# Kernel optimization log

Hardware: AMD Instinct MI355X
Metric: run time of the kernel (lower is better)

Reference implementation:

```python
import jax, jax.numpy as jnp
import numpy as np

GRID = 64
BIG = 1.0e6  # threshold pushing masked-out pixels to huge distance


def _grid_dist(grid_h, grid_w):
    # pairwise euclidean distance between all grid points, (H, W, H, W)
    xs, ys = jnp.meshgrid(jnp.arange(grid_h), jnp.arange(grid_w), indexing='ij')
    coords = jnp.stack([xs.ravel(), ys.ravel()], axis=-1).astype(jnp.float32)  # (H*W, 2)
    d = jnp.sqrt(jnp.sum((coords[:, None, :] - coords[None, :, :]) ** 2, axis=-1))
    return d.reshape(grid_h, grid_w, grid_h, grid_w)


def setup_inputs() -> dict:
    key = jax.random.key(0)
    k1, k2 = jax.random.split(key)
    gt = jax.random.uniform(k1, (8, 64, 64), dtype=jnp.float32)
    pred = jax.random.uniform(k2, (8, 64, 64), dtype=jnp.float32)
    return {"gt": gt, "pred": pred}


def reference(gt, pred):
    # mode='l2_sq': sum over last axis (W for a (B,H,W) mask), then mean
    loss = jnp.mean(jnp.sum((gt - pred) ** 2, axis=-1))

    # affinity loss (dist_mat += 1.0 as in the original)
    dist = _grid_dist(GRID, GRID) + 1.0  # (64,64,64,64)

    gt_th = gt + (1.0 - gt) * BIG      # (B,H,W)
    pred_th = pred + (1.0 - pred) * BIG

    # dist_masked[b,h,w,i,j] = gt_th[b,h,w] * dist[h,w,i,j] * pred[b,i,j]
    dist_masked = gt_th[:, :, :, None, None] * dist[None] * pred[:, None, None, :, :]
    min_dist = jnp.mean(jnp.min(dist_masked, axis=(3, 4)))

    dist_masked_inv = pred_th[:, :, :, None, None] * dist[None] * gt[:, None, None, :, :]
    min_dist_inv = jnp.mean(jnp.min(dist_masked_inv, axis=(3, 4)))

    return (loss, min_dist, min_dist_inv)
```

## Files before the change

### kernel.cpp

```cpp
#include <hip/hip_runtime.h>

#define BIGV 1.0e6f

__global__ __launch_bounds__(64) void imageloss_bnb(
    const float* __restrict__ gt, const float* __restrict__ pred,
    float* __restrict__ ws, float* __restrict__ out)
{
    __shared__ float img[4096];
    __shared__ float tmin[64];
    __shared__ int   order[64];
    __shared__ int   cnt9[16];

    const int blk   = blockIdx.x;
    const int patch = blk & 63;
    const int dir   = (blk >> 6) & 1;
    const int b     = blk >> 7;
    const int lane  = threadIdx.x;

    const float* __restrict__ src = (dir ? gt : pred) + b * 4096;

    #pragma unroll
    for (int k = 0; k < 16; ++k)
        ((float4*)img)[k * 64 + lane] = ((const float4*)src)[k * 64 + lane];
    if (lane < 16) cnt9[lane] = 0;
    __syncthreads();

    const int ti = lane >> 3, tj = lane & 7;
    {
        const float* tp = img + ti * 512 + tj * 8;
        float tv = 1e30f;
        #pragma unroll
        for (int r = 0; r < 8; ++r) {
            float4 a = *(const float4*)(tp + r * 64);
            float4 c = *(const float4*)(tp + r * 64 + 4);
            tv = fminf(tv, fminf(fminf(a.x, a.y), fminf(a.z, a.w)));
            tv = fminf(tv, fminf(fminf(c.x, c.y), fminf(c.z, c.w)));
        }
        tmin[lane] = tv;
    }

    const int Pi = patch >> 3, Pj = patch & 7;
    {
        int dti = ti - Pi; dti = dti < 0 ? -dti : dti;
        int dtj = tj - Pj; dtj = dtj < 0 ? -dtj : dtj;
        const int rho = dti > dtj ? dti : dtj;
        atomicAdd(&cnt9[rho], 1);
        __syncthreads();
        if (lane == 0) {
            int acc = 0;
            #pragma unroll
            for (int r = 0; r < 9; ++r) { int c = cnt9[r]; cnt9[r] = acc; acc += c; }
        }
        __syncthreads();
        const int slot = atomicAdd(&cnt9[rho], 1);
        order[slot] = lane;
    }
    __syncthreads();

    const int qi = Pi * 8 + (lane >> 3);
    const int qj = Pj * 8 + (lane & 7);
    const float qif = (float)qi, qjf = (float)qj;

    float ma = 3.4e38f, mb = 3.4e38f;

    for (int s = 0; s < 64; ++s) {
        const int t   = order[s];
        const int tti = t >> 3, ttj = t & 7;
        const float x0 = (float)(tti * 8), x1 = (float)(tti * 8 + 7);
        const float y0 = (float)(ttj * 8), y1 = (float)(ttj * 8 + 7);
        const float dx = fmaxf(fmaxf(x0 - qif, qif - x1), 0.0f);
        const float dy = fmaxf(fmaxf(y0 - qjf, qjf - y1), 0.0f);
        const float dbox = __builtin_amdgcn_sqrtf(fmaf(dx, dx, dy * dy));
        const float tm = tmin[t];
        const float bound = fmaf(tm, dbox, tm);
        if (__any(bound < fminf(ma, mb))) {
            const float* tpx = img + tti * 512 + ttj * 8;
            #pragma unroll
            for (int r = 0; r < 8; ++r) {
                const float4 va = *(const float4*)(tpx + r * 64);
                const float4 vb = *(const float4*)(tpx + r * 64 + 4);
                const float pif = (float)(tti * 8 + r);
                const float ddx = qif - pif;
                const float dx2 = ddx * ddx;
                #pragma unroll
                for (int cc = 0; cc < 4; ++cc) {
                    const float pjA = (float)(ttj * 8 + cc);
                    const float pjB = (float)(ttj * 8 + 4 + cc);
                    const float dyA = qjf - pjA;
                    const float dyB = qjf - pjB;
                    const float dA = __builtin_amdgcn_sqrtf(fmaf(dyA, dyA, dx2));
                    const float dB = __builtin_amdgcn_sqrtf(fmaf(dyB, dyB, dx2));
                    const float vA = (&va.x)[cc], vB = (&vb.x)[cc];
                    ma = fminf(ma, fmaf(vA, dA, vA));
                    mb = fminf(mb, fmaf(vB, dB, vB));
                }
            }
        }
    }
    const float m = fminf(ma, mb);

    const int cell = b * 4096 + qi * 64 + qj;
    const float own = img[qi * 64 + qj];

    float c12, sq = 0.0f;
    if (dir == 0) {
        const float g = gt[cell];
        const float gth = g + (1.0f - g) * BIGV;
        c12 = gth * m;
        const float df = g - own;
        sq = df * df;
    } else {
        const float p = pred[cell];
        const float pth = p + (1.0f - p) * BIGV;
        c12 = pth * m;
    }

    #pragma unroll
    for (int off = 32; off > 0; off >>= 1) {
        c12 += __shfl_down(c12, off, 64);
        sq  += __shfl_down(sq,  off, 64);
    }
    if (lane == 0) {
        if (dir == 0) {
            atomicAdd(&ws[0], sq);
            atomicAdd(&ws[1], c12);
        } else {
            atomicAdd(&ws[2], c12);
        }
        __threadfence();
        const int old = atomicAdd((int*)&ws[3], 1);
        if (old == 1023) {
            const float s0 = atomicAdd(&ws[0], 0.0f);
            const float s1 = atomicAdd(&ws[1], 0.0f);
            const float s2 = atomicAdd(&ws[2], 0.0f);
            out[0] = s0 * (1.0f / 512.0f);
            out[1] = s1 * (1.0f / 32768.0f);
            out[2] = s2 * (1.0f / 32768.0f);
        }
    }
}

extern "C" void kernel_launch(void* const* d_in, const int* in_sizes, int n_in,
                              void* d_out, int out_size, void* d_ws, size_t ws_size,
                              hipStream_t stream)
{
    const float* gt   = (const float*)d_in[0];
    const float* pred = (const float*)d_in[1];
    float* out = (float*)d_out;
    float* ws  = (float*)d_ws;

    hipMemsetAsync(ws, 0, 4 * sizeof(float), stream);
    imageloss_bnb<<<1024, 64, 0, stream>>>(gt, pred, ws, out);
}
```

Measured before the change: 53.77 us.

## Replace shared-memory tile ordering with ballot-based branch-and-bound pruning

Removes the LDS histogram/atomic sort of tiles by Chebyshev ring and the per-tile shared bound lookups. The kernel now always evaluates the 3x3 neighborhood tiles unconditionally, then uses a wave-wide max of current minima and ballot masks to prune farther tiles ring by ring, re-ballotting after each tile. Tile data is preloaded into registers per tile to increase ILP. The pruning uses the wave maximum instead of per-lane checks, which prunes more conservatively per tile, and it adds register pressure and extra cross-lane reductions.

```diff
diff --git a/kernel.cpp b/kernel.cpp
--- a/kernel.cpp
+++ b/kernel.cpp
@@ -2,14 +2,18 @@
 
 #define BIGV 1.0e6f
 
-__global__ __launch_bounds__(64) void imageloss_bnb(
+__device__ __forceinline__ float wave_max64(float v) {
+    #pragma unroll
+    for (int s = 32; s > 0; s >>= 1)
+        v = fmaxf(v, __shfl_xor(v, s, 64));
+    return v;
+}
+
+__global__ __launch_bounds__(64) void imageloss_bnb2(
     const float* __restrict__ gt, const float* __restrict__ pred,
     float* __restrict__ ws, float* __restrict__ out)
 {
     __shared__ float img[4096];
-    __shared__ float tmin[64];
-    __shared__ int   order[64];
-    __shared__ int   cnt9[16];
 
     const int blk   = blockIdx.x;
     const int patch = blk & 63;
@@ -22,79 +26,89 @@
     #pragma unroll
     for (int k = 0; k < 16; ++k)
         ((float4*)img)[k * 64 + lane] = ((const float4*)src)[k * 64 + lane];
-    if (lane < 16) cnt9[lane] = 0;
     __syncthreads();
 
     const int ti = lane >> 3, tj = lane & 7;
+    float tmin_l;
     {
         const float* tp = img + ti * 512 + tj * 8;
-        float tv = 1e30f;
+        float t0 = 1e30f, t1 = 1e30f;
         #pragma unroll
         for (int r = 0; r < 8; ++r) {
             float4 a = *(const float4*)(tp + r * 64);
             float4 c = *(const float4*)(tp + r * 64 + 4);
-            tv = fminf(tv, fminf(fminf(a.x, a.y), fminf(a.z, a.w)));
-            tv = fminf(tv, fminf(fminf(c.x, c.y), fminf(c.z, c.w)));
+            t0 = fminf(t0, fminf(fminf(a.x, a.y), fminf(a.z, a.w)));
+            t1 = fminf(t1, fminf(fminf(c.x, c.y), fminf(c.z, c.w)));
         }
-        tmin[lane] = tv;
+        tmin_l = fminf(t0, t1);
     }
 
     const int Pi = patch >> 3, Pj = patch & 7;
-    {
-        int dti = ti - Pi; dti = dti < 0 ? -dti : dti;
-        int dtj = tj - Pj; dtj = dtj < 0 ? -dtj : dtj;
-        const int rho = dti > dtj ? dti : dtj;
-        atomicAdd(&cnt9[rho], 1);
-        __syncthreads();
-        if (lane == 0) {
-            int acc = 0;
-            #pragma unroll
-            for (int r = 0; r < 9; ++r) { int c = cnt9[r]; cnt9[r] = acc; acc += c; }
-        }
-        __syncthreads();
-        const int slot = atomicAdd(&cnt9[rho], 1);
-        order[slot] = lane;
-    }
-    __syncthreads();
-
     const int qi = Pi * 8 + (lane >> 3);
     const int qj = Pj * 8 + (lane & 7);
     const float qif = (float)qi, qjf = (float)qj;
 
     float ma = 3.4e38f, mb = 3.4e38f;
 
-    for (int s = 0; s < 64; ++s) {
-        const int t   = order[s];
-        const int tti = t >> 3, ttj = t & 7;
-        const float x0 = (float)(tti * 8), x1 = (float)(tti * 8 + 7);
-        const float y0 = (float)(ttj * 8), y1 = (float)(ttj * 8 + 7);
-        const float dx = fmaxf(fmaxf(x0 - qif, qif - x1), 0.0f);
-        const float dy = fmaxf(fmaxf(y0 - qjf, qjf - y1), 0.0f);
-        const float dbox = __builtin_amdgcn_sqrtf(fmaf(dx, dx, dy * dy));
-        const float tm = tmin[t];
-        const float bound = fmaf(tm, dbox, tm);
-        if (__any(bound < fminf(ma, mb))) {
-            const float* tpx = img + tti * 512 + ttj * 8;
+    auto eval_tile = [&](int tti, int ttj) {
+        const float* tpx = img + tti * 512 + ttj * 8;
+        float4 va[8], vb[8];
+        #pragma unroll
+        for (int r = 0; r < 8; ++r) {
+            va[r] = *(const float4*)(tpx + r * 64);
+            vb[r] = *(const float4*)(tpx + r * 64 + 4);
+        }
+        #pragma unroll
+        for (int r = 0; r < 8; ++r) {
+            const float ddx = qif - (float)(tti * 8 + r);
+            const float dx2 = ddx * ddx;
             #pragma unroll
-            for (int r = 0; r < 8; ++r) {
-                const float4 va = *(const float4*)(tpx + r * 64);
-                const float4 vb = *(const float4*)(tpx + r * 64 + 4);
-                const float pif = (float)(tti * 8 + r);
-                const float ddx = qif - pif;
-                const float dx2 = ddx * ddx;
-                #pragma unroll
-                for (int cc = 0; cc < 4; ++cc) {
-                    const float pjA = (float)(ttj * 8 + cc);
-                    const float pjB = (float)(ttj * 8 + 4 + cc);
-                    const float dyA = qjf - pjA;
-                    const float dyB = qjf - pjB;
-                    const float dA = __builtin_amdgcn_sqrtf(fmaf(dyA, dyA, dx2));
-                    const float dB = __builtin_amdgcn_sqrtf(fmaf(dyB, dyB, dx2));
-                    const float vA = (&va.x)[cc], vB = (&vb.x)[cc];
-                    ma = fminf(ma, fmaf(vA, dA, vA));
-                    mb = fminf(mb, fmaf(vB, dB, vB));
-                }
+            for (int cc = 0; cc < 4; ++cc) {
+                const float dyA = qjf - (float)(ttj * 8 + cc);
+                const float dyB = qjf - (float)(ttj * 8 + 4 + cc);
+                const float dA = __builtin_amdgcn_sqrtf(fmaf(dyA, dyA, dx2));
+                const float dB = __builtin_amdgcn_sqrtf(fmaf(dyB, dyB, dx2));
+                const float vA = (&va[r].x)[cc], vB = (&vb[r].x)[cc];
+                ma = fminf(ma, fmaf(vA, dA, vA));
+                mb = fminf(mb, fmaf(vB, dB, vB));
             }
+        }
+    };
+
+    unsigned long long nearmask = 0;
+    #pragma unroll
+    for (int di = -1; di <= 1; ++di) {
+        #pragma unroll
+        for (int dj = -1; dj <= 1; ++dj) {
+            const int t2i = Pi + di, t2j = Pj + dj;
+            if ((unsigned)t2i < 8u && (unsigned)t2j < 8u) {
+                nearmask |= 1ull << (t2i * 8 + t2j);
+                eval_tile(t2i, t2j);
+            }
+        }
+    }
+
+    int adti = ti - Pi; adti = adti < 0 ? -adti : adti;
+    int adtj = tj - Pj; adtj = adtj < 0 ? -adtj : adtj;
+    const int rho_l = adti > adtj ? adti : adtj;
+    const float gx = fmaxf((float)(adti * 8 - 7), 0.0f);
+    const float gy = fmaxf((float)(adtj * 8 - 7), 0.0f);
+    const float dbox = __builtin_amdgcn_sqrtf(fmaf(gx, gx, gy * gy));
+    const float bnd = fmaf(tmin_l, dbox, tmin_l);
+
+    float M = wave_max64(fminf(ma, mb));
+    unsigned long long remaining = __ballot(bnd < M) & ~nearmask;
+
+    for (int rho = 2; rho <= 7 && remaining; ++rho) {
+        unsigned long long cur = remaining & __ballot(rho_l == rho);
+        while (cur) {
+            const int t = (int)__builtin_ctzll(cur);
+            const unsigned long long bit = 1ull << t;
+            cur &= ~bit; remaining &= ~bit;
+            eval_tile(t >> 3, t & 7);
+            M = wave_max64(fminf(ma, mb));
+            const unsigned long long alive = __ballot(bnd < M);
+            cur &= alive; remaining &= alive;
         }
     }
     const float m = fminf(ma, mb);
@@ -150,5 +164,5 @@
     float* ws  = (float*)d_ws;
 
     hipMemsetAsync(ws, 0, 4 * sizeof(float), stream);
-    imageloss_bnb<<<1024, 64, 0, stream>>>(gt, pred, ws, out);
+    imageloss_bnb2<<<1024, 64, 0, stream>>>(gt, pred, ws, out);
 }
```

New measurement: 48.74 us. 1.1x faster.
